# Kernel optimization log

Measured on AMD Instinct MI355X. Metric: run time of the kernel, lower is better.

Reference implementation:

```python
import jax, jax.numpy as jnp
import numpy as np
from jax import lax

B, IN_OCT, OUT_OCT, H, W, K = 16, 8, 16, 128, 128, 3
PAD = 1


def setup_inputs() -> dict:
    key = jax.random.key(0)
    k1, k2, k3 = jax.random.split(key, 3)
    x = jax.random.normal(k1, (B, IN_OCT * 8, H, W), dtype=jnp.float32)
    weight = jax.random.normal(k2, (OUT_OCT, IN_OCT, 8, 8, K, K), dtype=jnp.float32)
    bias = jax.random.normal(k3, (OUT_OCT, 8), dtype=jnp.float32)
    return {"x": x, "weight": weight, "bias": bias}


def reference(x, weight, bias):
    # weight: (out_oct, in_oct, p=8, q=8, kH, kW)
    # out[i, p] = sum_{j, q} conv2d(x[j, q], weight[i, j, p, q]) + bias[i, p]
    out_oct, in_oct = weight.shape[0], weight.shape[1]
    kh, kw = weight.shape[4], weight.shape[5]
    # -> (out_oct*8, in_oct*8, kH, kW) fused dense conv kernel
    w = jnp.transpose(weight, (0, 2, 1, 3, 4, 5)).reshape(out_oct * 8, in_oct * 8, kh, kw)
    out = lax.conv_general_dilated(
        x, w,
        window_strides=(1, 1),
        padding=((PAD, PAD), (PAD, PAD)),
        dimension_numbers=("NCHW", "OIHW", "NCHW"),
    )
    out = out + bias.reshape(-1)[None, :, None, None]
    return out
```

## Files before the change

### kernel.cpp

```cpp
#include <hip/hip_runtime.h>


#define B_    16
#define CIN   64
#define COUT  128
#define H_    128
#define W_    128
#define HW    (H_*W_)

typedef __attribute__((ext_vector_type(8))) short  short8;
typedef __attribute__((ext_vector_type(4))) float  f32x4;

#define XROW 128
#define XKH  (132*XROW)
#define XLDS_BYTES (3*XKH)

static __device__ __forceinline__ unsigned short f2bf(float f) {
    union { float f; unsigned int u; } c; c.f = f;
    unsigned int u = c.u;
    return (unsigned short)((u + 0x7fffu + ((u >> 16) & 1u)) >> 16);
}

__global__ void prep_weights(const float* __restrict__ wgt, unsigned short* __restrict__ warr) {
    int t = blockIdx.x * 256 + threadIdx.x;
    if (t >= 18*8*64) return;
    int lane = t & 63, ntg = (t >> 6) & 7, s = t >> 9;
    int tap = s >> 1, half = s & 1;
    int kh = tap / 3, kw = tap % 3;
    int oc = ntg*16 + (lane & 15);
    int c0 = half*32 + (lane >> 4)*8;
    const float* wp = wgt + (oc >> 3)*4608 + (c0 >> 3)*576 + (oc & 7)*72 + kh*3 + kw;
    short8 v;
#pragma unroll
    for (int j = 0; j < 8; ++j) v[j] = (short)f2bf(wp[j*9]);
    *(short8*)(warr + (size_t)t*8) = v;
}

#define ASTEP(S, BCUR, BNXT) do {                                               \
    const int kh_ = ((S) >> 1) / 3, kw_ = ((S) >> 1) % 3, hf_ = (S) & 1;        \
    short8 af[4];                                                               \
    _Pragma("unroll")                                                           \
    for (int mt = 0; mt < 4; ++mt)                                              \
        af[mt] = *(const short8*)(xl + (abase[kw_][hf_] + kh_*XKH + mt*2048));  \
    if ((S) + 2 < 18) {                                                         \
        _Pragma("unroll")                                                       \
        for (int nt = 0; nt < 4; ++nt)                                          \
            BNXT[nt] = wf[(((S)+2)*8 + nt)*64];                                 \
    }                                                                           \
    _Pragma("unroll")                                                           \
    for (int mt = 0; mt < 4; ++mt) {                                            \
        _Pragma("unroll")                                                       \
        for (int nt = 0; nt < 4; ++nt)                                          \
            acc[mt][nt] = __builtin_amdgcn_mfma_f32_16x16x32_bf16(              \
                af[mt], BCUR[nt], acc[mt][nt], 0, 0, 0);                        \
    }                                                                           \
} while (0)

__global__ __launch_bounds__(256, 2)
void conv_mfma(const float* __restrict__ x, const unsigned short* __restrict__ warr,
               const float* __restrict__ bias, float* __restrict__ out) {
    __shared__ __align__(16) unsigned char xl[XLDS_BYTES];

    int bid = blockIdx.x;
    int swz = (bid & 7)*256 + (bid >> 3);
    int b = swz >> 7, h = swz & 127;

    const int tid = threadIdx.x;

#pragma unroll
    for (int it = 0; it < 12; ++it) {
        int idx = it*256 + tid;
        int wc  = idx & 127;
        int cg  = (idx >> 7) & 7;
        int kh  = idx >> 10;
        int hh  = h - 1 + kh;
        bool hok = (unsigned)hh < (unsigned)H_;
        const float* xp = x + (size_t)b*CIN*HW + (size_t)cg*8*HW + hh*W_ + wc;
        short8 pk;
#pragma unroll
        for (int j = 0; j < 8; ++j)
            pk[j] = (short)f2bf(hok ? xp[j*HW] : 0.0f);
        int wp = wc + 1;
        int byte = kh*XKH + wp*XROW + ((cg*16) ^ ((wp & 7) << 4));
        *(short8*)(xl + byte) = pk;
    }
    if (tid < 48) {
        int cg = tid & 7, e = (tid >> 3) & 1, kh = tid >> 4;
        int wp = e ? 129 : 0;
        int byte = kh*XKH + wp*XROW + ((cg*16) ^ ((wp & 7) << 4));
        short8 z = {0,0,0,0,0,0,0,0};
        *(short8*)(xl + byte) = z;
    }
    __syncthreads();

    const int lane = tid & 63;
    const int wid  = tid >> 6;
    const int lw = lane & 15, hi = lane >> 4;
    const int wave_m = wid >> 1, wave_n = wid & 1;
    const int wl = wave_m*64 + lw;

    int abase[3][2];
#pragma unroll
    for (int kw = 0; kw < 3; ++kw) {
        int wp0 = wl + kw;
        int sw  = (wp0 & 7) << 4;
#pragma unroll
        for (int half = 0; half < 2; ++half)
            abase[kw][half] = wp0*XROW + ((half*64 + hi*16) ^ sw);
    }

    const short8* wf = ((const short8*)warr) + (size_t)(wave_n*4)*64 + lane;

    f32x4 acc[4][4] = {};
    short8 bf0[4], bf1[4], bf2[4];
#pragma unroll
    for (int nt = 0; nt < 4; ++nt) {
        bf0[nt] = wf[(0*8 + nt)*64];
        bf1[nt] = wf[(1*8 + nt)*64];
    }

    ASTEP(0,  bf0, bf2); ASTEP(1,  bf1, bf0); ASTEP(2,  bf2, bf1);
    ASTEP(3,  bf0, bf2); ASTEP(4,  bf1, bf0); ASTEP(5,  bf2, bf1);
    ASTEP(6,  bf0, bf2); ASTEP(7,  bf1, bf0); ASTEP(8,  bf2, bf1);
    ASTEP(9,  bf0, bf2); ASTEP(10, bf1, bf0); ASTEP(11, bf2, bf1);
    ASTEP(12, bf0, bf2); ASTEP(13, bf1, bf0); ASTEP(14, bf2, bf1);
    ASTEP(15, bf0, bf2); ASTEP(16, bf1, bf0); ASTEP(17, bf2, bf1);

    float bv[4];
#pragma unroll
    for (int nt = 0; nt < 4; ++nt) bv[nt] = bias[wave_n*64 + nt*16 + lw];

    const size_t obase = (size_t)b*COUT*HW + (size_t)h*W_;
#pragma unroll
    for (int mt = 0; mt < 4; ++mt) {
#pragma unroll
        for (int nt = 0; nt < 4; ++nt) {
            int oc = wave_n*64 + nt*16 + lw;
            int w0 = wave_m*64 + mt*16 + hi*4;
            f32x4 v = acc[mt][nt];
            v += bv[nt];
            *(f32x4*)(out + obase + (size_t)oc*HW + w0) = v;
        }
    }
}

extern "C" void kernel_launch(void* const* d_in, const int* in_sizes, int n_in,
                              void* d_out, int out_size, void* d_ws, size_t ws_size,
                              hipStream_t stream) {
    const float* x    = (const float*)d_in[0];
    const float* wgt  = (const float*)d_in[1];
    const float* bias = (const float*)d_in[2];
    float* out = (float*)d_out;
    unsigned short* warr = (unsigned short*)d_ws;

    prep_weights<<<36, 256, 0, stream>>>(wgt, warr);
    conv_mfma<<<2048, 256, 0, stream>>>(x, warr, bias, out);
}
```

Measured before the change: 232.2 us.

## Compute two output rows per block to share the halo input rows

Each block now has 512 threads and produces two output rows, staging four input rows in LDS instead of three per row. This cuts the redundant global loads and bf16 conversions of the halo rows from 3x to 2x. The weight register prefetch also shrinks from double lookahead to single to lower register pressure, and launch bounds are raised to 512 threads with 4 waves per EU. LDS per block grows to about 67KB, which may limit occupancy, and the shorter weight prefetch exposes more latency.

```diff
diff --git a/kernel.cpp b/kernel.cpp
--- a/kernel.cpp
+++ b/kernel.cpp
@@ -13,7 +13,7 @@
 
 #define XROW 128
 #define XKH  (132*XROW)
-#define XLDS_BYTES (3*XKH)
+#define XLDS_BYTES (4*XKH)
 
 static __device__ __forceinline__ unsigned short f2bf(float f) {
     union { float f; unsigned int u; } c; c.f = f;
@@ -42,10 +42,10 @@
     _Pragma("unroll")                                                           \
     for (int mt = 0; mt < 4; ++mt)                                              \
         af[mt] = *(const short8*)(xl + (abase[kw_][hf_] + kh_*XKH + mt*2048));  \
-    if ((S) + 2 < 18) {                                                         \
+    if ((S) + 1 < 18) {                                                         \
         _Pragma("unroll")                                                       \
         for (int nt = 0; nt < 4; ++nt)                                          \
-            BNXT[nt] = wf[(((S)+2)*8 + nt)*64];                                 \
+            BNXT[nt] = wf[(((S)+1)*8 + nt)*64];                                 \
     }                                                                           \
     _Pragma("unroll")                                                           \
     for (int mt = 0; mt < 4; ++mt) {                                            \
@@ -56,38 +56,40 @@
     }                                                                           \
 } while (0)
 
-__global__ __launch_bounds__(256, 2)
+__global__ __launch_bounds__(512, 4)
 void conv_mfma(const float* __restrict__ x, const unsigned short* __restrict__ warr,
                const float* __restrict__ bias, float* __restrict__ out) {
     __shared__ __align__(16) unsigned char xl[XLDS_BYTES];
 
     int bid = blockIdx.x;
-    int swz = (bid & 7)*256 + (bid >> 3);
-    int b = swz >> 7, h = swz & 127;
+    int swz = (bid & 7)*128 + (bid >> 3);
+    int b  = swz >> 6;
+    int h0 = (swz & 63)*2;
 
     const int tid = threadIdx.x;
 
 #pragma unroll
-    for (int it = 0; it < 12; ++it) {
-        int idx = it*256 + tid;
-        int wc  = idx & 127;
-        int cg  = (idx >> 7) & 7;
-        int kh  = idx >> 10;
-        int hh  = h - 1 + kh;
-        bool hok = (unsigned)hh < (unsigned)H_;
-        const float* xp = x + (size_t)b*CIN*HW + (size_t)cg*8*HW + hh*W_ + wc;
+    for (int it = 0; it < 8; ++it) {
+        const int xr = it >> 1;
+        const int cg = (it & 1)*4 + (tid >> 7);
+        const int wc = tid & 127;
+        const int hh = h0 - 1 + xr;
         short8 pk;
+        if ((unsigned)hh < (unsigned)H_) {
+            const float* xp = x + (size_t)b*CIN*HW + (size_t)cg*8*HW + hh*W_ + wc;
 #pragma unroll
-        for (int j = 0; j < 8; ++j)
-            pk[j] = (short)f2bf(hok ? xp[j*HW] : 0.0f);
-        int wp = wc + 1;
-        int byte = kh*XKH + wp*XROW + ((cg*16) ^ ((wp & 7) << 4));
+            for (int j = 0; j < 8; ++j) pk[j] = (short)f2bf(xp[j*HW]);
+        } else {
+            pk = (short8){0,0,0,0,0,0,0,0};
+        }
+        const int wp = wc + 1;
+        const int byte = xr*XKH + wp*XROW + ((cg*16) ^ ((wp & 7) << 4));
         *(short8*)(xl + byte) = pk;
     }
-    if (tid < 48) {
-        int cg = tid & 7, e = (tid >> 3) & 1, kh = tid >> 4;
-        int wp = e ? 129 : 0;
-        int byte = kh*XKH + wp*XROW + ((cg*16) ^ ((wp & 7) << 4));
+    if (tid < 64) {
+        const int cg = tid & 7, e = (tid >> 3) & 1, xr = tid >> 4;
+        const int wp = e ? 129 : 0;
+        const int byte = xr*XKH + wp*XROW + ((cg*16) ^ ((wp & 7) << 4));
         short8 z = {0,0,0,0,0,0,0,0};
         *(short8*)(xl + byte) = z;
     }
@@ -96,50 +98,49 @@
     const int lane = tid & 63;
     const int wid  = tid >> 6;
     const int lw = lane & 15, hi = lane >> 4;
-    const int wave_m = wid >> 1, wave_n = wid & 1;
-    const int wl = wave_m*64 + lw;
+    const int wave_n = wid & 1, wave_m = wid >> 1;
+    const int row_sel = wave_m >> 1;
+    const int wcol = (wave_m & 1)*64;
+    const int wl = wcol + lw;
 
     int abase[3][2];
 #pragma unroll
     for (int kw = 0; kw < 3; ++kw) {
-        int wp0 = wl + kw;
-        int sw  = (wp0 & 7) << 4;
+        const int wp0 = wl + kw;
+        const int sw  = (wp0 & 7) << 4;
 #pragma unroll
         for (int half = 0; half < 2; ++half)
-            abase[kw][half] = wp0*XROW + ((half*64 + hi*16) ^ sw);
+            abase[kw][half] = row_sel*XKH + wp0*XROW + ((half*64 + hi*16) ^ sw);
     }
 
     const short8* wf = ((const short8*)warr) + (size_t)(wave_n*4)*64 + lane;
 
     f32x4 acc[4][4] = {};
-    short8 bf0[4], bf1[4], bf2[4];
+    short8 ba[4], bb[4];
 #pragma unroll
-    for (int nt = 0; nt < 4; ++nt) {
-        bf0[nt] = wf[(0*8 + nt)*64];
-        bf1[nt] = wf[(1*8 + nt)*64];
-    }
+    for (int nt = 0; nt < 4; ++nt) ba[nt] = wf[nt*64];
 
-    ASTEP(0,  bf0, bf2); ASTEP(1,  bf1, bf0); ASTEP(2,  bf2, bf1);
-    ASTEP(3,  bf0, bf2); ASTEP(4,  bf1, bf0); ASTEP(5,  bf2, bf1);
-    ASTEP(6,  bf0, bf2); ASTEP(7,  bf1, bf0); ASTEP(8,  bf2, bf1);
-    ASTEP(9,  bf0, bf2); ASTEP(10, bf1, bf0); ASTEP(11, bf2, bf1);
-    ASTEP(12, bf0, bf2); ASTEP(13, bf1, bf0); ASTEP(14, bf2, bf1);
-    ASTEP(15, bf0, bf2); ASTEP(16, bf1, bf0); ASTEP(17, bf2, bf1);
+    ASTEP(0,  ba, bb); ASTEP(1,  bb, ba); ASTEP(2,  ba, bb);
+    ASTEP(3,  bb, ba); ASTEP(4,  ba, bb); ASTEP(5,  bb, ba);
+    ASTEP(6,  ba, bb); ASTEP(7,  bb, ba); ASTEP(8,  ba, bb);
+    ASTEP(9,  bb, ba); ASTEP(10, ba, bb); ASTEP(11, bb, ba);
+    ASTEP(12, ba, bb); ASTEP(13, bb, ba); ASTEP(14, ba, bb);
+    ASTEP(15, bb, ba); ASTEP(16, ba, bb); ASTEP(17, bb, ba);
 
     float bv[4];
 #pragma unroll
     for (int nt = 0; nt < 4; ++nt) bv[nt] = bias[wave_n*64 + nt*16 + lw];
 
-    const size_t obase = (size_t)b*COUT*HW + (size_t)h*W_;
+    const int hh_out = h0 + row_sel;
 #pragma unroll
     for (int mt = 0; mt < 4; ++mt) {
 #pragma unroll
         for (int nt = 0; nt < 4; ++nt) {
-            int oc = wave_n*64 + nt*16 + lw;
-            int w0 = wave_m*64 + mt*16 + hi*4;
+            const int oc = wave_n*64 + nt*16 + lw;
+            const int w0 = wcol + mt*16 + hi*4;
             f32x4 v = acc[mt][nt];
             v += bv[nt];
-            *(f32x4*)(out + obase + (size_t)oc*HW + w0) = v;
+            *(f32x4*)(out + (size_t)b*COUT*HW + (size_t)oc*HW + hh_out*W_ + w0) = v;
         }
     }
 }
@@ -154,5 +155,5 @@
     unsigned short* warr = (unsigned short*)d_ws;
 
     prep_weights<<<36, 256, 0, stream>>>(wgt, warr);
-    conv_mfma<<<2048, 256, 0, stream>>>(x, warr, bias, out);
+    conv_mfma<<<1024, 512, 0, stream>>>(x, warr, bias, out);
 }
```

Measured after the change: 216.6 us. 1.07x faster.
